# Kernel optimization log

Measured on AMD Instinct MI355X. Metric: run time of the kernel, lower is better.

Reference implementation:

```python
import jax, jax.numpy as jnp
import numpy as np

SIZE = 512
LANG_NUM = 8
B, S, D = 32, 2048, SIZE


def setup_inputs() -> dict:
    key = jax.random.key(0)
    ks = jax.random.split(key, 10)
    sc = 1.0 / np.sqrt(D)
    inp = {
        "old_x": jax.random.normal(ks[0], (B, S, D), jnp.float32),
        "x": jax.random.normal(ks[1], (B, S, D), jnp.float32),
        "lang": jax.random.randint(ks[2], (B,), 0, LANG_NUM, jnp.int32),
        # shared linear (no bias): y = x @ W.T
        "share_W": jax.random.uniform(ks[3], (D, D), jnp.float32, -sc, sc),
        # per-language expert linears (no bias)
        "langs_W": jax.random.uniform(ks[4], (LANG_NUM, D, D), jnp.float32, -sc, sc),
        # per-language gate: layer1 (D->D with bias), layer2 (D->1 with bias)
        "gate_W1": jax.random.uniform(ks[5], (LANG_NUM, D, D), jnp.float32, -sc, sc),
        "gate_b1": jax.random.uniform(ks[6], (LANG_NUM, D), jnp.float32, -sc, sc),
        "gate_W2": jax.random.uniform(ks[7], (LANG_NUM, D), jnp.float32, -sc, sc),
        "gate_b2": jax.random.uniform(ks[8], (LANG_NUM,), jnp.float32, -sc, sc),
    }
    return inp


def reference(old_x, x, lang, share_W, langs_W, gate_W1, gate_b1, gate_W2, gate_b2):
    # shared path: [B,S,D] @ [D,D].T
    share_h = jnp.einsum("bsd,ed->bse", x, share_W)
    # gather per-sample expert weights by lang index
    Wl = langs_W[lang]            # [B,D,D]
    W1 = gate_W1[lang]            # [B,D,D]
    b1 = gate_b1[lang]            # [B,D]
    W2 = gate_W2[lang]            # [B,D]
    b2 = gate_b2[lang]            # [B]
    langs_h = jnp.einsum("bsd,bed->bse", x, Wl)
    # GateLayer on old_x: relu(L1(x)) + x -> L2 -> sigmoid
    h = jax.nn.relu(jnp.einsum("bsd,bed->bse", old_x, W1) + b1[:, None, :]) + old_x
    gate_logit = jnp.einsum("bsd,bd->bs", h, W2) + b2[:, None]
    gate_prob = jax.nn.sigmoid(gate_logit)[:, :, None]   # [B,S,1]
    return share_h * (1.0 - gate_prob) + langs_h * gate_prob
```

## Files before the change

### kernel.cpp

```cpp
#include <hip/hip_runtime.h>
#include <hip/hip_bf16.h>

#define B_ 32
#define S_ 2048
#define D_ 512

typedef __attribute__((ext_vector_type(8))) short bf16x8;
typedef __attribute__((ext_vector_type(4))) float f32x4;
typedef unsigned short ushort_t;

__device__ __forceinline__ float b2f(ushort_t u) {
  union { unsigned int i; float f; } v; v.i = ((unsigned int)u) << 16; return v.f;
}
__device__ __forceinline__ ushort_t f2b(float f) {
  union { float f; unsigned int i; } v; v.f = f;
  return (ushort_t)((v.i + 0x7FFFu + ((v.i >> 16) & 1u)) >> 16);
}

__device__ __forceinline__ f32x4 mfma16(bf16x8 a, bf16x8 b, f32x4 c) {
  return __builtin_amdgcn_mfma_f32_16x16x32_bf16(a, b, c, 0, 0, 0);
}

__global__ void detect_kernel(const unsigned int* __restrict__ w, int* __restrict__ flag) {
  __shared__ int cnt;
  if (threadIdx.x == 0) cnt = 0;
  __syncthreads();
  int c = 0;
  #pragma unroll
  for (int i = 0; i < 4; ++i) {
    unsigned int v = w[threadIdx.x + i * 256];
    unsigned int e = (v >> 7) & 0xFFu;
    if (e >= 110u && e <= 140u) ++c;
  }
  atomicAdd(&cnt, c);
  __syncthreads();
  if (threadIdx.x == 0) flag[0] = (cnt > 512) ? 1 : 0;
}

template <int DT>
__device__ __forceinline__ float ldf(const void* p, size_t idx) {
  if constexpr (DT == 0) return ((const float*)p)[idx];
  else                   return b2f(((const ushort_t*)p)[idx]);
}

template <int DT>
__device__ __forceinline__ void stage_tile(const void* gv, size_t elem_off,
                                           ushort_t* tile, int tid) {
  const int row = tid >> 1, half = tid & 1;
  const size_t base = elem_off + (size_t)row * D_ + half * 16;
  bf16x8 ch0, ch1;
  if constexpr (DT == 0) {
    const float4* src = (const float4*)((const float*)gv + base);
    float4 a = src[0], b = src[1], c = src[2], d = src[3];
    ushort_t t[16];
    t[0] = f2b(a.x); t[1] = f2b(a.y); t[2]  = f2b(a.z); t[3]  = f2b(a.w);
    t[4] = f2b(b.x); t[5] = f2b(b.y); t[6]  = f2b(b.z); t[7]  = f2b(b.w);
    t[8] = f2b(c.x); t[9] = f2b(c.y); t[10] = f2b(c.z); t[11] = f2b(c.w);
    t[12] = f2b(d.x); t[13] = f2b(d.y); t[14] = f2b(d.z); t[15] = f2b(d.w);
    ch0 = *(const bf16x8*)t; ch1 = *(const bf16x8*)(t + 8);
  } else {
    const bf16x8* src = (const bf16x8*)((const ushort_t*)gv + base);
    ch0 = src[0]; ch1 = src[1];
  }
  const int swz = (row >> 1) & 3;
  const int c0 = half * 2, c1 = c0 + 1;
  *(bf16x8*)(tile + row * 32 + ((c0 ^ swz) << 3)) = ch0;
  *(bf16x8*)(tile + row * 32 + ((c1 ^ swz) << 3)) = ch1;
}

__device__ __forceinline__ bf16x8 read_frag(const ushort_t* tile, int row, int quad) {
  int g = quad ^ ((row >> 1) & 3);
  return *(const bf16x8*)(tile + row * 32 + g * 8);
}

template <int DT>
__global__ __launch_bounds__(256, 2)
void gate_kernel(const void* __restrict__ old_x, const int* __restrict__ lang,
                 const void* __restrict__ W1, const void* __restrict__ b1,
                 const void* __restrict__ W2, const void* __restrict__ b2,
                 const int* __restrict__ flag, float* __restrict__ gate) {
  if (flag[0] != DT) return;
  const int b    = blockIdx.y;
  const int s0   = blockIdx.x * 128;
  const int tid  = threadIdx.x;
  const int wave = tid >> 6, lane = tid & 63, quad = lane >> 4, ln = lane & 15;
  const int m_off = (wave >> 1) * 64, n_off = (wave & 1) * 64;
  const int lg = lang[b];

  __shared__ __align__(16) ushort_t As[128 * 32];
  __shared__ __align__(16) ushort_t Bs[128 * 32];
  __shared__ float b1s[512], w2s[512], logit[128];

  for (int i = tid; i < 512; i += 256) {
    b1s[i] = ldf<DT>(b1, (size_t)lg * 512 + i);
    w2s[i] = ldf<DT>(W2, (size_t)lg * 512 + i);
  }
  if (tid < 128) logit[tid] = 0.f;
  __syncthreads();

  {
    const int row = tid >> 1, half = tid & 1;
    const size_t off = ((size_t)b * S_ + s0 + row) * D_ + half * 256;
    float ex = 0.f;
    if constexpr (DT == 0) {
      const float4* xr = (const float4*)((const float*)old_x + off);
      #pragma unroll 8
      for (int c = 0; c < 64; ++c) {
        float4 v = xr[c];
        const float* wp = &w2s[half * 256 + c * 4];
        ex += v.x * wp[0] + v.y * wp[1] + v.z * wp[2] + v.w * wp[3];
      }
    } else {
      const ushort_t* xr = (const ushort_t*)old_x + off;
      #pragma unroll 4
      for (int c = 0; c < 32; ++c) {
        bf16x8 v = *(const bf16x8*)(xr + c * 8);
        #pragma unroll
        for (int j = 0; j < 8; ++j)
          ex += b2f((ushort_t)v[j]) * w2s[half * 256 + c * 8 + j];
      }
    }
    atomicAdd(&logit[row], ex);
  }

  const size_t Aoff = ((size_t)b * S_ + s0) * D_;
  float logacc[16];
  #pragma unroll
  for (int i = 0; i < 16; ++i) logacc[i] = 0.f;

  for (int et = 0; et < 4; ++et) {
    const int e0 = et * 128;
    const size_t Boff = ((size_t)lg * D_ + e0) * D_;
    f32x4 acc[16];
    #pragma unroll
    for (int i = 0; i < 16; ++i) { f32x4 z = {0.f, 0.f, 0.f, 0.f}; acc[i] = z; }

    for (int k0 = 0; k0 < D_; k0 += 32) {
      __syncthreads();
      stage_tile<DT>(old_x, Aoff + k0, As, tid);
      stage_tile<DT>(W1,   Boff + k0, Bs, tid);
      __syncthreads();
      bf16x8 af[4], bfr[4];
      #pragma unroll
      for (int mf = 0; mf < 4; ++mf) af[mf]  = read_frag(As, m_off + mf * 16 + ln, quad);
      #pragma unroll
      for (int nf = 0; nf < 4; ++nf) bfr[nf] = read_frag(Bs, n_off + nf * 16 + ln, quad);
      #pragma unroll
      for (int mf = 0; mf < 4; ++mf)
        #pragma unroll
        for (int nf = 0; nf < 4; ++nf)
          acc[mf * 4 + nf] = mfma16(af[mf], bfr[nf], acc[mf * 4 + nf]);
    }
    #pragma unroll
    for (int nf = 0; nf < 4; ++nf) {
      int e = e0 + n_off + nf * 16 + ln;
      float b1v = b1s[e], w2v = w2s[e];
      #pragma unroll
      for (int mf = 0; mf < 4; ++mf)
        #pragma unroll
        for (int r = 0; r < 4; ++r) {
          float v = acc[mf * 4 + nf][r] + b1v;
          logacc[mf * 4 + r] += fmaxf(v, 0.f) * w2v;
        }
    }
  }

  #pragma unroll
  for (int off = 1; off < 16; off <<= 1)
    #pragma unroll
    for (int i = 0; i < 16; ++i)
      logacc[i] += __shfl_xor(logacc[i], off, 64);
  if (ln == 0) {
    #pragma unroll
    for (int mf = 0; mf < 4; ++mf)
      #pragma unroll
      for (int r = 0; r < 4; ++r)
        atomicAdd(&logit[m_off + mf * 16 + quad * 4 + r], logacc[mf * 4 + r]);
  }
  __syncthreads();
  if (tid < 128) {
    float b2v = ldf<DT>(b2, lg);
    float l = logit[tid] + b2v;
    gate[(size_t)b * S_ + s0 + tid] = 1.f / (1.f + expf(-l));
  }
}

template <int DT>
__global__ __launch_bounds__(256, 2)
void out_kernel(const void* __restrict__ x, const int* __restrict__ lang,
                const void* __restrict__ shareW, const void* __restrict__ langsW,
                const float* __restrict__ gate, const int* __restrict__ flag,
                void* __restrict__ out) {
  if (flag[0] != DT) return;
  const int b    = blockIdx.z;
  const int s0   = blockIdx.y * 128;
  const int e0   = blockIdx.x * 128;
  const int tid  = threadIdx.x;
  const int wave = tid >> 6, lane = tid & 63, quad = lane >> 4, ln = lane & 15;
  const int m_off = (wave >> 1) * 64, n_off = (wave & 1) * 64;
  const int lg = lang[b];

  __shared__ __align__(16) ushort_t As[128 * 32];
  __shared__ __align__(16) ushort_t Ss[128 * 32];
  __shared__ __align__(16) ushort_t Ls[128 * 32];

  const size_t Aoff = ((size_t)b * S_ + s0) * D_;
  const size_t Soff = (size_t)e0 * D_;
  const size_t Loff = ((size_t)lg * D_ + e0) * D_;

  f32x4 accS[16], accL[16];
  #pragma unroll
  for (int i = 0; i < 16; ++i) {
    f32x4 z = {0.f, 0.f, 0.f, 0.f};
    accS[i] = z; accL[i] = z;
  }

  for (int k0 = 0; k0 < D_; k0 += 32) {
    __syncthreads();
    stage_tile<DT>(x,      Aoff + k0, As, tid);
    stage_tile<DT>(shareW, Soff + k0, Ss, tid);
    stage_tile<DT>(langsW, Loff + k0, Ls, tid);
    __syncthreads();
    bf16x8 af[4], sf[4], lf[4];
    #pragma unroll
    for (int mf = 0; mf < 4; ++mf) af[mf] = read_frag(As, m_off + mf * 16 + ln, quad);
    #pragma unroll
    for (int nf = 0; nf < 4; ++nf) {
      sf[nf] = read_frag(Ss, n_off + nf * 16 + ln, quad);
      lf[nf] = read_frag(Ls, n_off + nf * 16 + ln, quad);
    }
    #pragma unroll
    for (int mf = 0; mf < 4; ++mf)
      #pragma unroll
      for (int nf = 0; nf < 4; ++nf) {
        accS[mf * 4 + nf] = mfma16(af[mf], sf[nf], accS[mf * 4 + nf]);
        accL[mf * 4 + nf] = mfma16(af[mf], lf[nf], accL[mf * 4 + nf]);
      }
  }

  #pragma unroll
  for (int mf = 0; mf < 4; ++mf) {
    int srow = s0 + m_off + mf * 16 + quad * 4;
    float gv[4];
    #pragma unroll
    for (int r = 0; r < 4; ++r) gv[r] = gate[(size_t)b * S_ + srow + r];
    #pragma unroll
    for (int nf = 0; nf < 4; ++nf) {
      int col = e0 + n_off + nf * 16 + ln;
      f32x4 cs = accS[mf * 4 + nf], cl = accL[mf * 4 + nf];
      #pragma unroll
      for (int r = 0; r < 4; ++r) {
        float v = cs[r] + gv[r] * (cl[r] - cs[r]);
        size_t idx = ((size_t)b * S_ + srow + r) * D_ + col;
        if constexpr (DT == 0) ((float*)out)[idx] = v;
        else                   ((ushort_t*)out)[idx] = f2b(v);
      }
    }
  }
}

extern "C" void kernel_launch(void* const* d_in, const int* in_sizes, int n_in,
                              void* d_out, int out_size, void* d_ws, size_t ws_size,
                              hipStream_t stream) {
  const void* old_x  = d_in[0];
  const void* x      = d_in[1];
  const int*  lang   = (const int*)d_in[2];
  const void* shareW = d_in[3];
  const void* langsW = d_in[4];
  const void* gW1    = d_in[5];
  const void* gb1    = d_in[6];
  const void* gW2    = d_in[7];
  const void* gb2    = d_in[8];

  float* gate = (float*)d_ws;
  int*   flag = (int*)((char*)d_ws + (size_t)B_ * S_ * sizeof(float));

  detect_kernel<<<1, 256, 0, stream>>>((const unsigned int*)old_x, flag);

  dim3 g1(S_ / 128, B_);
  gate_kernel<0><<<g1, dim3(256), 0, stream>>>(old_x, lang, gW1, gb1, gW2, gb2, flag, gate);
  gate_kernel<1><<<g1, dim3(256), 0, stream>>>(old_x, lang, gW1, gb1, gW2, gb2, flag, gate);

  dim3 g2(D_ / 128, S_ / 128, B_);
  out_kernel<0><<<g2, dim3(256), 0, stream>>>(x, lang, shareW, langsW, gate, flag, d_out);
  out_kernel<1><<<g2, dim3(256), 0, stream>>>(x, lang, shareW, langsW, gate, flag, d_out);
}
```

Baseline: 556.2 us.

## Double-buffer GEMM tiles, widen gate kernel, swizzle block order, merge dtype variants

Both GEMM kernels now use double-buffered LDS tiles, issuing the next K-step's global loads into registers before the MFMAs and writing them to LDS after, with one barrier per step. The gate kernel uses 512 threads computing all 512 output columns per block, so old_x is staged once instead of four times. The residual dot product with W2 is folded into the staged tiles rather than re-reading old_x. Other changes: block index swizzling for L2 locality, nontemporal output stores, and a single launch per kernel that branches on the dtype flag instead of two launches. The trade is higher LDS and register use, which may lower occupancy.

Measured after the change: 550.4 us. No clear change (-1.0%).

```diff
diff --git a/kernel.cpp b/kernel.cpp
--- a/kernel.cpp
+++ b/kernel.cpp
@@ -43,220 +43,334 @@
   else                   return b2f(((const ushort_t*)p)[idx]);
 }
 
-template <int DT>
-__device__ __forceinline__ void stage_tile(const void* gv, size_t elem_off,
-                                           ushort_t* tile, int tid) {
-  const int row = tid >> 1, half = tid & 1;
-  const size_t base = elem_off + (size_t)row * D_ + half * 16;
-  bf16x8 ch0, ch1;
-  if constexpr (DT == 0) {
-    const float4* src = (const float4*)((const float*)gv + base);
-    float4 a = src[0], b = src[1], c = src[2], d = src[3];
-    ushort_t t[16];
-    t[0] = f2b(a.x); t[1] = f2b(a.y); t[2]  = f2b(a.z); t[3]  = f2b(a.w);
-    t[4] = f2b(b.x); t[5] = f2b(b.y); t[6]  = f2b(b.z); t[7]  = f2b(b.w);
-    t[8] = f2b(c.x); t[9] = f2b(c.y); t[10] = f2b(c.z); t[11] = f2b(c.w);
-    t[12] = f2b(d.x); t[13] = f2b(d.y); t[14] = f2b(d.z); t[15] = f2b(d.w);
-    ch0 = *(const bf16x8*)t; ch1 = *(const bf16x8*)(t + 8);
-  } else {
-    const bf16x8* src = (const bf16x8*)((const ushort_t*)gv + base);
-    ch0 = src[0]; ch1 = src[1];
-  }
-  const int swz = (row >> 1) & 3;
-  const int c0 = half * 2, c1 = c0 + 1;
-  *(bf16x8*)(tile + row * 32 + ((c0 ^ swz) << 3)) = ch0;
-  *(bf16x8*)(tile + row * 32 + ((c1 ^ swz) << 3)) = ch1;
-}
-
 __device__ __forceinline__ bf16x8 read_frag(const ushort_t* tile, int row, int quad) {
   int g = quad ^ ((row >> 1) & 3);
   return *(const bf16x8*)(tile + row * 32 + g * 8);
 }
 
-template <int DT>
-__global__ __launch_bounds__(256, 2)
+
+template <int DT> struct TR16 { float4 f[4]; bf16x8 h[2]; };
+
+template <int DT>
+__device__ __forceinline__ void t16_load(const void* gv, size_t base, int tid, TR16<DT>& t) {
+  const int row = tid >> 1, half = tid & 1;
+  const size_t off = base + (size_t)row * D_ + half * 16;
+  if constexpr (DT == 0) {
+    const float4* s = (const float4*)((const float*)gv + off);
+    t.f[0] = s[0]; t.f[1] = s[1]; t.f[2] = s[2]; t.f[3] = s[3];
+  } else {
+    const bf16x8* s = (const bf16x8*)((const ushort_t*)gv + off);
+    t.h[0] = s[0]; t.h[1] = s[1];
+  }
+}
+template <int DT>
+__device__ __forceinline__ void t16_store(ushort_t* tile, int tid, const TR16<DT>& t) {
+  const int row = tid >> 1, half = tid & 1;
+  bf16x8 ch0, ch1;
+  if constexpr (DT == 0) {
+    ushort_t u[16];
+    u[0]  = f2b(t.f[0].x); u[1]  = f2b(t.f[0].y); u[2]  = f2b(t.f[0].z); u[3]  = f2b(t.f[0].w);
+    u[4]  = f2b(t.f[1].x); u[5]  = f2b(t.f[1].y); u[6]  = f2b(t.f[1].z); u[7]  = f2b(t.f[1].w);
+    u[8]  = f2b(t.f[2].x); u[9]  = f2b(t.f[2].y); u[10] = f2b(t.f[2].z); u[11] = f2b(t.f[2].w);
+    u[12] = f2b(t.f[3].x); u[13] = f2b(t.f[3].y); u[14] = f2b(t.f[3].z); u[15] = f2b(t.f[3].w);
+    ch0 = *(const bf16x8*)u; ch1 = *(const bf16x8*)(u + 8);
+  } else { ch0 = t.h[0]; ch1 = t.h[1]; }
+  const int swz = (row >> 1) & 3, c0 = half * 2;
+  *(bf16x8*)(tile + row * 32 + (((c0    ) ^ swz) << 3)) = ch0;
+  *(bf16x8*)(tile + row * 32 + (((c0 + 1) ^ swz) << 3)) = ch1;
+}
+
+template <int DT> struct TRA { float4 f[2]; bf16x8 h; };
+
+template <int DT>
+__device__ __forceinline__ void ta_load(const void* gv, size_t base, int tid, TRA<DT>& t) {
+  const int row = tid >> 2, g = tid & 3;
+  const size_t off = base + (size_t)row * D_ + g * 8;
+  if constexpr (DT == 0) {
+    const float4* s = (const float4*)((const float*)gv + off);
+    t.f[0] = s[0]; t.f[1] = s[1];
+  } else {
+    t.h = *(const bf16x8*)((const ushort_t*)gv + off);
+  }
+}
+template <int DT>
+__device__ __forceinline__ void ta_store(ushort_t* tile, int tid, const TRA<DT>& t) {
+  const int row = tid >> 2, g = tid & 3;
+  bf16x8 ch;
+  if constexpr (DT == 0) {
+    ushort_t u[8];
+    u[0] = f2b(t.f[0].x); u[1] = f2b(t.f[0].y); u[2] = f2b(t.f[0].z); u[3] = f2b(t.f[0].w);
+    u[4] = f2b(t.f[1].x); u[5] = f2b(t.f[1].y); u[6] = f2b(t.f[1].z); u[7] = f2b(t.f[1].w);
+    ch = *(const bf16x8*)u;
+  } else ch = t.h;
+  const int swz = (row >> 1) & 3;
+  *(bf16x8*)(tile + row * 32 + ((g ^ swz) << 3)) = ch;
+}
+
+template <int DT> struct TRB { float4 f[8]; bf16x8 h[4]; };
+
+template <int DT>
+__device__ __forceinline__ void tb_load(const void* gv, size_t base, int tid, TRB<DT>& t) {
+  const size_t off = base + (size_t)tid * D_;
+  if constexpr (DT == 0) {
+    const float4* s = (const float4*)((const float*)gv + off);
+    #pragma unroll
+    for (int i = 0; i < 8; ++i) t.f[i] = s[i];
+  } else {
+    const bf16x8* s = (const bf16x8*)((const ushort_t*)gv + off);
+    #pragma unroll
+    for (int i = 0; i < 4; ++i) t.h[i] = s[i];
+  }
+}
+template <int DT>
+__device__ __forceinline__ void tb_store(ushort_t* tile, int tid, const TRB<DT>& t) {
+  const int row = tid, swz = (row >> 1) & 3;
+  #pragma unroll
+  for (int g = 0; g < 4; ++g) {
+    bf16x8 ch;
+    if constexpr (DT == 0) {
+      ushort_t u[8];
+      float4 a = t.f[2 * g], b = t.f[2 * g + 1];
+      u[0] = f2b(a.x); u[1] = f2b(a.y); u[2] = f2b(a.z); u[3] = f2b(a.w);
+      u[4] = f2b(b.x); u[5] = f2b(b.y); u[6] = f2b(b.z); u[7] = f2b(b.w);
+      ch = *(const bf16x8*)u;
+    } else ch = t.h[g];
+    *(bf16x8*)(tile + row * 32 + ((g ^ swz) << 3)) = ch;
+  }
+}
+
+struct GateSmem {
+  alignas(16) ushort_t As[2][128 * 32];
+  alignas(16) ushort_t Bs[2][512 * 32];
+  float b1s[512], w2s[512], logit[128];
+};
+struct OutSmem {
+  alignas(16) ushort_t As[2][128 * 32];
+  alignas(16) ushort_t Ss[2][128 * 32];
+  alignas(16) ushort_t Ls[2][128 * 32];
+};
+
+template <int DT>
+__device__ __forceinline__ void gate_body(const void* __restrict__ old_x,
+    const int* __restrict__ lang, const void* __restrict__ W1,
+    const void* __restrict__ b1, const void* __restrict__ W2,
+    const void* __restrict__ b2p, float* __restrict__ gate, GateSmem& sm) {
+  int bid = blockIdx.y * gridDim.x + blockIdx.x;
+  int swz = (bid & 7) * 64 + (bid >> 3);
+  const int s0 = (swz & 15) * 128;
+  const int b  = swz >> 4;
+  const int tid  = threadIdx.x;
+  const int wave = tid >> 6, lane = tid & 63, quad = lane >> 4, ln = lane & 15;
+  const int m_off = (wave >> 2) * 64;
+  const int n_off = (wave & 3) * 128;
+  const int lg = lang[b];
+
+  sm.b1s[tid] = ldf<DT>(b1, (size_t)lg * 512 + tid);
+  sm.w2s[tid] = ldf<DT>(W2, (size_t)lg * 512 + tid);
+  if (tid < 128) sm.logit[tid] = 0.f;
+
+  const size_t Aoff = ((size_t)b * S_ + s0) * D_;
+  const size_t Boff = (size_t)lg * D_ * D_;
+
+  f32x4 acc[4][8];
+  #pragma unroll
+  for (int i = 0; i < 4; ++i)
+    #pragma unroll
+    for (int j = 0; j < 8; ++j) { f32x4 z = {0.f, 0.f, 0.f, 0.f}; acc[i][j] = z; }
+
+  TRA<DT> ta; TRB<DT> tb;
+  tb_load<DT>(W1, Boff, tid, tb);
+  ta_load<DT>(old_x, Aoff, tid, ta);
+  tb_store<DT>(sm.Bs[0], tid, tb);
+  ta_store<DT>(sm.As[0], tid, ta);
+  __syncthreads();
+
+  const int rrow  = tid >> 2, rg = tid & 3;
+  const int rslot = (rg ^ ((rrow >> 1) & 3)) << 3;
+  float res = 0.f;
+
+  for (int step = 0; step < 16; ++step) {
+    const int cur = step & 1;
+    if (step < 15) {
+      tb_load<DT>(W1, Boff + (step + 1) * 32, tid, tb);
+      ta_load<DT>(old_x, Aoff + (step + 1) * 32, tid, ta);
+    }
+    bf16x8 af[4];
+    #pragma unroll
+    for (int mf = 0; mf < 4; ++mf)
+      af[mf] = read_frag(sm.As[cur], m_off + mf * 16 + ln, quad);
+    {
+      bf16x8 rv = *(const bf16x8*)(sm.As[cur] + rrow * 32 + rslot);
+      #pragma unroll
+      for (int j = 0; j < 8; ++j)
+        res += b2f((ushort_t)rv[j]) * sm.w2s[step * 32 + rg * 8 + j];
+    }
+    #pragma unroll
+    for (int nh = 0; nh < 2; ++nh) {
+      bf16x8 bfr[4];
+      #pragma unroll
+      for (int nf = 0; nf < 4; ++nf)
+        bfr[nf] = read_frag(sm.Bs[cur], n_off + (nh * 4 + nf) * 16 + ln, quad);
+      #pragma unroll
+      for (int mf = 0; mf < 4; ++mf)
+        #pragma unroll
+        for (int nf = 0; nf < 4; ++nf)
+          acc[mf][nh * 4 + nf] = mfma16(af[mf], bfr[nf], acc[mf][nh * 4 + nf]);
+    }
+    if (step < 15) {
+      const int nxt = cur ^ 1;
+      tb_store<DT>(sm.Bs[nxt], tid, tb);
+      ta_store<DT>(sm.As[nxt], tid, ta);
+    }
+    __syncthreads();
+  }
+  atomicAdd(&sm.logit[rrow], res);
+
+  float logacc[16];
+  #pragma unroll
+  for (int i = 0; i < 16; ++i) logacc[i] = 0.f;
+  #pragma unroll
+  for (int nf = 0; nf < 8; ++nf) {
+    int e = n_off + nf * 16 + ln;
+    float b1v = sm.b1s[e], w2v = sm.w2s[e];
+    #pragma unroll
+    for (int mf = 0; mf < 4; ++mf)
+      #pragma unroll
+      for (int r = 0; r < 4; ++r) {
+        float v = acc[mf][nf][r] + b1v;
+        logacc[mf * 4 + r] += fmaxf(v, 0.f) * w2v;
+      }
+  }
+  #pragma unroll
+  for (int off = 1; off < 16; off <<= 1)
+    #pragma unroll
+    for (int i = 0; i < 16; ++i)
+      logacc[i] += __shfl_xor(logacc[i], off, 64);
+  if (ln == 0) {
+    #pragma unroll
+    for (int mf = 0; mf < 4; ++mf)
+      #pragma unroll
+      for (int r = 0; r < 4; ++r)
+        atomicAdd(&sm.logit[m_off + mf * 16 + quad * 4 + r], logacc[mf * 4 + r]);
+  }
+  __syncthreads();
+  if (tid < 128) {
+    float bb = ldf<DT>(b2p, lg);
+    float l = sm.logit[tid] + bb;
+    gate[(size_t)b * S_ + s0 + tid] = 1.f / (1.f + expf(-l));
+  }
+}
+
+__global__ __launch_bounds__(512, 2)
 void gate_kernel(const void* __restrict__ old_x, const int* __restrict__ lang,
                  const void* __restrict__ W1, const void* __restrict__ b1,
                  const void* __restrict__ W2, const void* __restrict__ b2,
                  const int* __restrict__ flag, float* __restrict__ gate) {
-  if (flag[0] != DT) return;
-  const int b    = blockIdx.y;
-  const int s0   = blockIdx.x * 128;
+  __shared__ GateSmem sm;
+  if (flag[0] == 0) gate_body<0>(old_x, lang, W1, b1, W2, b2, gate, sm);
+  else              gate_body<1>(old_x, lang, W1, b1, W2, b2, gate, sm);
+}
+
+template <int DT>
+__device__ __forceinline__ void out_body(const void* __restrict__ x,
+    const int* __restrict__ lang, const void* __restrict__ shareW,
+    const void* __restrict__ langsW, const float* __restrict__ gate,
+    void* __restrict__ out, OutSmem& sm) {
+  int bid = (blockIdx.z * gridDim.y + blockIdx.y) * gridDim.x + blockIdx.x;
+  int swz = (bid & 7) * 256 + (bid >> 3);
+  const int e0 = (swz & 3) * 128;
+  const int s0 = ((swz >> 2) & 15) * 128;
+  const int b  = swz >> 6;
   const int tid  = threadIdx.x;
   const int wave = tid >> 6, lane = tid & 63, quad = lane >> 4, ln = lane & 15;
   const int m_off = (wave >> 1) * 64, n_off = (wave & 1) * 64;
   const int lg = lang[b];
 
-  __shared__ __align__(16) ushort_t As[128 * 32];
-  __shared__ __align__(16) ushort_t Bs[128 * 32];
-  __shared__ float b1s[512], w2s[512], logit[128];
-
-  for (int i = tid; i < 512; i += 256) {
-    b1s[i] = ldf<DT>(b1, (size_t)lg * 512 + i);
-    w2s[i] = ldf<DT>(W2, (size_t)lg * 512 + i);
-  }
-  if (tid < 128) logit[tid] = 0.f;
-  __syncthreads();
-
-  {
-    const int row = tid >> 1, half = tid & 1;
-    const size_t off = ((size_t)b * S_ + s0 + row) * D_ + half * 256;
-    float ex = 0.f;
-    if constexpr (DT == 0) {
-      const float4* xr = (const float4*)((const float*)old_x + off);
-      #pragma unroll 8
-      for (int c = 0; c < 64; ++c) {
-        float4 v = xr[c];
-        const float* wp = &w2s[half * 256 + c * 4];
-        ex += v.x * wp[0] + v.y * wp[1] + v.z * wp[2] + v.w * wp[3];
+  const size_t Aoff = ((size_t)b * S_ + s0) * D_;
+  const size_t Soff = (size_t)e0 * D_;
+  const size_t Loff = ((size_t)lg * D_ + e0) * D_;
+
+  f32x4 accS[4][4], accL[4][4];
+  #pragma unroll
+  for (int i = 0; i < 4; ++i)
+    #pragma unroll
+    for (int j = 0; j < 4; ++j) {
+      f32x4 z = {0.f, 0.f, 0.f, 0.f};
+      accS[i][j] = z; accL[i][j] = z;
+    }
+
+  TR16<DT> ta, ts, tl;
+  t16_load<DT>(shareW, Soff, tid, ts);
+  t16_load<DT>(langsW, Loff, tid, tl);
+  t16_load<DT>(x,      Aoff, tid, ta);
+  t16_store<DT>(sm.Ss[0], tid, ts);
+  t16_store<DT>(sm.Ls[0], tid, tl);
+  t16_store<DT>(sm.As[0], tid, ta);
+  __syncthreads();
+
+  for (int step = 0; step < 16; ++step) {
+    const int cur = step & 1;
+    if (step < 15) {
+      t16_load<DT>(shareW, Soff + (step + 1) * 32, tid, ts);
+      t16_load<DT>(langsW, Loff + (step + 1) * 32, tid, tl);
+      t16_load<DT>(x,      Aoff + (step + 1) * 32, tid, ta);
+    }
+    bf16x8 af[4], sf[4], lf[4];
+    #pragma unroll
+    for (int mf = 0; mf < 4; ++mf)
+      af[mf] = read_frag(sm.As[cur], m_off + mf * 16 + ln, quad);
+    #pragma unroll
+    for (int nf = 0; nf < 4; ++nf) {
+      sf[nf] = read_frag(sm.Ss[cur], n_off + nf * 16 + ln, quad);
+      lf[nf] = read_frag(sm.Ls[cur], n_off + nf * 16 + ln, quad);
+    }
+    #pragma unroll
+    for (int mf = 0; mf < 4; ++mf)
+      #pragma unroll
+      for (int nf = 0; nf < 4; ++nf) {
+        accS[mf][nf] = mfma16(af[mf], sf[nf], accS[mf][nf]);
+        accL[mf][nf] = mfma16(af[mf], lf[nf], accL[mf][nf]);
       }
-    } else {
-      const ushort_t* xr = (const ushort_t*)old_x + off;
-      #pragma unroll 4
-      for (int c = 0; c < 32; ++c) {
-        bf16x8 v = *(const bf16x8*)(xr + c * 8);
-        #pragma unroll
-        for (int j = 0; j < 8; ++j)
-          ex += b2f((ushort_t)v[j]) * w2s[half * 256 + c * 8 + j];
+    if (step < 15) {
+      const int nxt = cur ^ 1;
+      t16_store<DT>(sm.Ss[nxt], tid, ts);
+      t16_store<DT>(sm.Ls[nxt], tid, tl);
+      t16_store<DT>(sm.As[nxt], tid, ta);
+    }
+    __syncthreads();
+  }
+
+  #pragma unroll
+  for (int mf = 0; mf < 4; ++mf) {
+    int srow = s0 + m_off + mf * 16 + quad * 4;
+    float gv[4];
+    #pragma unroll
+    for (int r = 0; r < 4; ++r) gv[r] = gate[(size_t)b * S_ + srow + r];
+    #pragma unroll
+    for (int nf = 0; nf < 4; ++nf) {
+      int col = e0 + n_off + nf * 16 + ln;
+      f32x4 cs = accS[mf][nf], cl = accL[mf][nf];
+      #pragma unroll
+      for (int r = 0; r < 4; ++r) {
+        float v = cs[r] + gv[r] * (cl[r] - cs[r]);
+        size_t idx = ((size_t)b * S_ + srow + r) * D_ + col;
+        if constexpr (DT == 0)
+          __builtin_nontemporal_store(v, (float*)out + idx);
+        else
+          __builtin_nontemporal_store(f2b(v), (ushort_t*)out + idx);
       }
     }
-    atomicAdd(&logit[row], ex);
-  }
-
-  const size_t Aoff = ((size_t)b * S_ + s0) * D_;
-  float logacc[16];
-  #pragma unroll
-  for (int i = 0; i < 16; ++i) logacc[i] = 0.f;
-
-  for (int et = 0; et < 4; ++et) {
-    const int e0 = et * 128;
-    const size_t Boff = ((size_t)lg * D_ + e0) * D_;
-    f32x4 acc[16];
-    #pragma unroll
-    for (int i = 0; i < 16; ++i) { f32x4 z = {0.f, 0.f, 0.f, 0.f}; acc[i] = z; }
-
-    for (int k0 = 0; k0 < D_; k0 += 32) {
-      __syncthreads();
-      stage_tile<DT>(old_x, Aoff + k0, As, tid);
-      stage_tile<DT>(W1,   Boff + k0, Bs, tid);
-      __syncthreads();
-      bf16x8 af[4], bfr[4];
-      #pragma unroll
-      for (int mf = 0; mf < 4; ++mf) af[mf]  = read_frag(As, m_off + mf * 16 + ln, quad);
-      #pragma unroll
-      for (int nf = 0; nf < 4; ++nf) bfr[nf] = read_frag(Bs, n_off + nf * 16 + ln, quad);
-      #pragma unroll
-      for (int mf = 0; mf < 4; ++mf)
-        #pragma unroll
-        for (int nf = 0; nf < 4; ++nf)
-          acc[mf * 4 + nf] = mfma16(af[mf], bfr[nf], acc[mf * 4 + nf]);
-    }
-    #pragma unroll
-    for (int nf = 0; nf < 4; ++nf) {
-      int e = e0 + n_off + nf * 16 + ln;
-      float b1v = b1s[e], w2v = w2s[e];
-      #pragma unroll
-      for (int mf = 0; mf < 4; ++mf)
-        #pragma unroll
-        for (int r = 0; r < 4; ++r) {
-          float v = acc[mf * 4 + nf][r] + b1v;
-          logacc[mf * 4 + r] += fmaxf(v, 0.f) * w2v;
-        }
-    }
-  }
-
-  #pragma unroll
-  for (int off = 1; off < 16; off <<= 1)
-    #pragma unroll
-    for (int i = 0; i < 16; ++i)
-      logacc[i] += __shfl_xor(logacc[i], off, 64);
-  if (ln == 0) {
-    #pragma unroll
-    for (int mf = 0; mf < 4; ++mf)
-      #pragma unroll
-      for (int r = 0; r < 4; ++r)
-        atomicAdd(&logit[m_off + mf * 16 + quad * 4 + r], logacc[mf * 4 + r]);
-  }
-  __syncthreads();
-  if (tid < 128) {
-    float b2v = ldf<DT>(b2, lg);
-    float l = logit[tid] + b2v;
-    gate[(size_t)b * S_ + s0 + tid] = 1.f / (1.f + expf(-l));
-  }
-}
-
-template <int DT>
+  }
+}
+
 __global__ __launch_bounds__(256, 2)
 void out_kernel(const void* __restrict__ x, const int* __restrict__ lang,
                 const void* __restrict__ shareW, const void* __restrict__ langsW,
                 const float* __restrict__ gate, const int* __restrict__ flag,
                 void* __restrict__ out) {
-  if (flag[0] != DT) return;
-  const int b    = blockIdx.z;
-  const int s0   = blockIdx.y * 128;
-  const int e0   = blockIdx.x * 128;
-  const int tid  = threadIdx.x;
-  const int wave = tid >> 6, lane = tid & 63, quad = lane >> 4, ln = lane & 15;
-  const int m_off = (wave >> 1) * 64, n_off = (wave & 1) * 64;
-  const int lg = lang[b];
-
-  __shared__ __align__(16) ushort_t As[128 * 32];
-  __shared__ __align__(16) ushort_t Ss[128 * 32];
-  __shared__ __align__(16) ushort_t Ls[128 * 32];
-
-  const size_t Aoff = ((size_t)b * S_ + s0) * D_;
-  const size_t Soff = (size_t)e0 * D_;
-  const size_t Loff = ((size_t)lg * D_ + e0) * D_;
-
-  f32x4 accS[16], accL[16];
-  #pragma unroll
-  for (int i = 0; i < 16; ++i) {
-    f32x4 z = {0.f, 0.f, 0.f, 0.f};
-    accS[i] = z; accL[i] = z;
-  }
-
-  for (int k0 = 0; k0 < D_; k0 += 32) {
-    __syncthreads();
-    stage_tile<DT>(x,      Aoff + k0, As, tid);
-    stage_tile<DT>(shareW, Soff + k0, Ss, tid);
-    stage_tile<DT>(langsW, Loff + k0, Ls, tid);
-    __syncthreads();
-    bf16x8 af[4], sf[4], lf[4];
-    #pragma unroll
-    for (int mf = 0; mf < 4; ++mf) af[mf] = read_frag(As, m_off + mf * 16 + ln, quad);
-    #pragma unroll
-    for (int nf = 0; nf < 4; ++nf) {
-      sf[nf] = read_frag(Ss, n_off + nf * 16 + ln, quad);
-      lf[nf] = read_frag(Ls, n_off + nf * 16 + ln, quad);
-    }
-    #pragma unroll
-    for (int mf = 0; mf < 4; ++mf)
-      #pragma unroll
-      for (int nf = 0; nf < 4; ++nf) {
-        accS[mf * 4 + nf] = mfma16(af[mf], sf[nf], accS[mf * 4 + nf]);
-        accL[mf * 4 + nf] = mfma16(af[mf], lf[nf], accL[mf * 4 + nf]);
-      }
-  }
-
-  #pragma unroll
-  for (int mf = 0; mf < 4; ++mf) {
-    int srow = s0 + m_off + mf * 16 + quad * 4;
-    float gv[4];
-    #pragma unroll
-    for (int r = 0; r < 4; ++r) gv[r] = gate[(size_t)b * S_ + srow + r];
-    #pragma unroll
-    for (int nf = 0; nf < 4; ++nf) {
-      int col = e0 + n_off + nf * 16 + ln;
-      f32x4 cs = accS[mf * 4 + nf], cl = accL[mf * 4 + nf];
-      #pragma unroll
-      for (int r = 0; r < 4; ++r) {
-        float v = cs[r] + gv[r] * (cl[r] - cs[r]);
-        size_t idx = ((size_t)b * S_ + srow + r) * D_ + col;
-        if constexpr (DT == 0) ((float*)out)[idx] = v;
-        else                   ((ushort_t*)out)[idx] = f2b(v);
-      }
-    }
-  }
+  __shared__ OutSmem sm;
+  if (flag[0] == 0) out_body<0>(x, lang, shareW, langsW, gate, out, sm);
+  else              out_body<1>(x, lang, shareW, langsW, gate, out, sm);
 }
 
 extern "C" void kernel_launch(void* const* d_in, const int* in_sizes, int n_in,
@@ -278,10 +392,8 @@
   detect_kernel<<<1, 256, 0, stream>>>((const unsigned int*)old_x, flag);
 
   dim3 g1(S_ / 128, B_);
-  gate_kernel<0><<<g1, dim3(256), 0, stream>>>(old_x, lang, gW1, gb1, gW2, gb2, flag, gate);
-  gate_kernel<1><<<g1, dim3(256), 0, stream>>>(old_x, lang, gW1, gb1, gW2, gb2, flag, gate);
+  gate_kernel<<<g1, dim3(512), 0, stream>>>(old_x, lang, gW1, gb1, gW2, gb2, flag, gate);
 
   dim3 g2(D_ / 128, S_ / 128, B_);
-  out_kernel<0><<<g2, dim3(256), 0, stream>>>(x, lang, shareW, langsW, gate, flag, d_out);
-  out_kernel<1><<<g2, dim3(256), 0, stream>>>(x, lang, shareW, langsW, gate, flag, d_out);
-}
+  out_kernel<<<g2, dim3(256), 0, stream>>>(x, lang, shareW, langsW, gate, flag, d_out);
+}
```
